# Performance work log

Measured on AMD Instinct MI355X. Metric: run time of the kernel, lower is better.

## Reference

```python
import jax, jax.numpy as jnp
import numpy as np

BN_EPS = 1e-5


def setup_inputs() -> dict:
    key = jax.random.key(0)
    k0, k1, kw, kb, kg, kbe = jax.random.split(key, 6)
    N, L0, L1, D, H = 2, 512, 512, 128, 64
    z0 = jax.random.normal(k0, (N, L0, D), dtype=jnp.float32)
    z1 = jax.random.normal(k1, (N, L1, D), dtype=jnp.float32)
    # Conv2d(2D, H, 1) weight (H, 2D, 1, 1) -> stored as (H, 2D); PyTorch kaiming-uniform-ish init
    bound = 1.0 / np.sqrt(2 * D)
    conv_w = jax.random.uniform(kw, (H, 2 * D), minval=-bound, maxval=bound, dtype=jnp.float32)
    conv_b = jax.random.uniform(kb, (H,), minval=-bound, maxval=bound, dtype=jnp.float32)
    bn_gamma = jnp.ones((H,), dtype=jnp.float32)
    bn_beta = jnp.zeros((H,), dtype=jnp.float32)
    return {"z0": z0, "z1": z1, "conv_w": conv_w, "conv_b": conv_b,
            "bn_gamma": bn_gamma, "bn_beta": bn_beta}


def reference(z0, z1, conv_w, conv_b, bn_gamma, bn_beta):
    # z0: (N, L0, D), z1: (N, L1, D)
    z0t = jnp.transpose(z0, (0, 2, 1))  # (N, D, L0)
    z1t = jnp.transpose(z1, (0, 2, 1))  # (N, D, L1)
    a = z0t[:, :, :, None]              # (N, D, L0, 1)
    b = z1t[:, :, None, :]              # (N, D, 1, L1)
    z_dif = jnp.abs(a - b)              # (N, D, L0, L1)
    z_mul = a * b                       # (N, D, L0, L1)
    z_cat = jnp.concatenate([z_dif, z_mul], axis=1)  # (N, 2D, L0, L1)
    # 1x1 conv == channel contraction
    y = jnp.einsum('ncxy,hc->nhxy', z_cat, conv_w) + conv_b[None, :, None, None]
    y = jax.nn.elu(y)
    # BatchNorm2d, training mode (batch statistics over N, L0, L1 per channel)
    mean = jnp.mean(y, axis=(0, 2, 3), keepdims=True)
    var = jnp.var(y, axis=(0, 2, 3), keepdims=True)
    y = (y - mean) * jax.lax.rsqrt(var + BN_EPS)
    y = y * bn_gamma[None, :, None, None] + bn_beta[None, :, None, None]
    return y
```

## Files before the change

kernel.cpp:

```cpp
#include <hip/hip_runtime.h>

#define NBATCH 2
#define LL 512
#define DDIM 128
#define HCH 64
#define NBLOCKS 1024

typedef float f32x4 __attribute__((ext_vector_type(4)));
typedef __bf16 bf16x8 __attribute__((ext_vector_type(8)));

__device__ __forceinline__ float elu_f(float v) {
  return v > 0.0f ? v : (__expf(v) - 1.0f);
}

__global__ void wprep_kernel(const float* __restrict__ w, bf16x8* __restrict__ wf) {
  int s = blockIdx.x * 256 + threadIdx.x;
  int ck = s >> 8;
  int rem = s & 255;
  int ht = rem >> 6;
  int l = rem & 63;
  int h = ht * 16 + (l & 15);
  int c = ck * 32 + ((l >> 4) << 3);
  const float* src = w + h * 256 + c;
  bf16x8 v;
#pragma unroll
  for (int j = 0; j < 8; ++j) v[j] = (__bf16)src[j];
  wf[s] = v;
}

__device__ __forceinline__ int swz(int i) { return i ^ ((i >> 4) & 7); }

template <int PASS>
__global__ __launch_bounds__(256, 2) void fused_kernel(
    const float* __restrict__ z0g, const float* __restrict__ z1g,
    const bf16x8* __restrict__ wf, const float* __restrict__ cb,
    const float* __restrict__ sstab, float* __restrict__ partials,
    float* __restrict__ out) {
  __shared__ float z0_lds[16 * 128];
  __shared__ f32x4 z1f[1024];
  __shared__ float sred[128];
  __shared__ float cb_lds[64];
  __shared__ float sc_lds[128];

  const int t = threadIdx.x;
  const int lane = t & 63;
  const int wv = t >> 6;
  const int bid = blockIdx.x;
  const int by = bid & 15, bx = (bid >> 4) & 31, n = bid >> 9;
  const int x0 = bx * 16, y0 = by * 32;

  {
    int r = t >> 4, cs = t & 15;
    const f32x4* g0 = (const f32x4*)(z0g + (size_t)(n * LL + x0 + r) * DDIM + cs * 8);
    f32x4 a0 = g0[0], a1 = g0[1];
    ((f32x4*)z0_lds)[r * 32 + cs * 2 + 0] = a0;
    ((f32x4*)z0_lds)[r * 32 + cs * 2 + 1] = a1;
#pragma unroll
    for (int s = t; s < 512; s += 256) {
      int rr = s >> 4, cs1 = s & 15;
      const f32x4* g1 = (const f32x4*)(z1g + (size_t)(n * LL + y0 + rr) * DDIM + cs1 * 8);
      f32x4 b0 = g1[0], b1 = g1[1];
      int yt = rr >> 4, rl = rr & 15, ck = cs1 >> 2, gg = cs1 & 3, fl = gg * 16 + rl;
      int i0 = ((0 * 2 + yt) * 4 + ck) * 64 + fl;
      int i1 = ((1 * 2 + yt) * 4 + ck) * 64 + fl;
      z1f[swz(i0)] = b0;
      z1f[swz(i1)] = b1;
    }
    if (t < 128) sred[t] = 0.0f;
    if (t < 64) cb_lds[t] = cb[t];
    if (PASS == 1 && t < 128) sc_lds[t] = sstab[t];
  }
  __syncthreads();

  f32x4 acc[4][4][2];
  const f32x4 zero4 = {0.f, 0.f, 0.f, 0.f};
#pragma unroll
  for (int xi = 0; xi < 4; ++xi)
#pragma unroll
    for (int ht = 0; ht < 4; ++ht)
#pragma unroll
      for (int yt = 0; yt < 2; ++yt) acc[xi][ht][yt] = zero4;

#pragma unroll
  for (int ckz = 0; ckz < 4; ++ckz) {
    bf16x8 afd[4], afm[4];
#pragma unroll
    for (int ht = 0; ht < 4; ++ht) {
      afd[ht] = wf[(ckz * 4 + ht) * 64 + lane];
      afm[ht] = wf[((ckz + 4) * 4 + ht) * 64 + lane];
    }
    f32x4 b0[2], b1[2];
#pragma unroll
    for (int yt = 0; yt < 2; ++yt) {
      b0[yt] = z1f[swz(((0 * 2 + yt) * 4 + ckz) * 64 + lane)];
      b1[yt] = z1f[swz(((1 * 2 + yt) * 4 + ckz) * 64 + lane)];
    }
#pragma unroll
    for (int xi = 0; xi < 4; ++xi) {
      const int xl = wv * 4 + xi;
      const f32x4* z0p = (const f32x4*)&z0_lds[xl * 128 + ckz * 32 + ((lane >> 4) << 3)];
      f32x4 a0 = z0p[0], a1 = z0p[1];
#pragma unroll
      for (int yt = 0; yt < 2; ++yt) {
        bf16x8 bd, bm;
#pragma unroll
        for (int j = 0; j < 4; ++j) {
          bd[j] = (__bf16)fabsf(a0[j] - b0[yt][j]);
          bd[4 + j] = (__bf16)fabsf(a1[j] - b1[yt][j]);
          bm[j] = (__bf16)(a0[j] * b0[yt][j]);
          bm[4 + j] = (__bf16)(a1[j] * b1[yt][j]);
        }
#pragma unroll
        for (int ht = 0; ht < 4; ++ht) {
          acc[xi][ht][yt] =
              __builtin_amdgcn_mfma_f32_16x16x32_bf16(afd[ht], bd, acc[xi][ht][yt], 0, 0, 0);
          acc[xi][ht][yt] =
              __builtin_amdgcn_mfma_f32_16x16x32_bf16(afm[ht], bm, acc[xi][ht][yt], 0, 0, 0);
        }
      }
    }
  }

  if (PASS == 0) {
    float s1[4][4], s2[4][4];
#pragma unroll
    for (int ht = 0; ht < 4; ++ht)
#pragma unroll
      for (int i = 0; i < 4; ++i) { s1[ht][i] = 0.f; s2[ht][i] = 0.f; }
#pragma unroll
    for (int xi = 0; xi < 4; ++xi)
#pragma unroll
      for (int ht = 0; ht < 4; ++ht)
#pragma unroll
        for (int yt = 0; yt < 2; ++yt)
#pragma unroll
          for (int i = 0; i < 4; ++i) {
            int h = ht * 16 + ((lane >> 4) << 2) + i;
            float v = elu_f(acc[xi][ht][yt][i] + cb_lds[h]);
            s1[ht][i] += v;
            s2[ht][i] += v * v;
          }
#pragma unroll
    for (int ht = 0; ht < 4; ++ht)
#pragma unroll
      for (int i = 0; i < 4; ++i) {
#pragma unroll
        for (int m = 1; m <= 8; m <<= 1) {
          s1[ht][i] += __shfl_xor(s1[ht][i], m, 64);
          s2[ht][i] += __shfl_xor(s2[ht][i], m, 64);
        }
        if ((lane & 15) == 0) {
          int h = ht * 16 + ((lane >> 4) << 2) + i;
          atomicAdd(&sred[h], s1[ht][i]);
          atomicAdd(&sred[64 + h], s2[ht][i]);
        }
      }
    __syncthreads();
    if (t < 128) partials[(size_t)bid * 128 + t] = sred[t];
  } else {
#pragma unroll
    for (int xi = 0; xi < 4; ++xi) {
      const int x = x0 + wv * 4 + xi;
#pragma unroll
      for (int ht = 0; ht < 4; ++ht)
#pragma unroll
        for (int i = 0; i < 4; ++i) {
          int h = ht * 16 + ((lane >> 4) << 2) + i;
          float sc = sc_lds[h], sh = sc_lds[64 + h];
          float* p = out + ((size_t)(n * HCH + h) * LL + x) * LL + y0 + (lane & 15);
          float v0 = elu_f(acc[xi][ht][0][i] + cb_lds[h]);
          float v1 = elu_f(acc[xi][ht][1][i] + cb_lds[h]);
          p[0] = v0 * sc + sh;
          p[16] = v1 * sc + sh;
        }
    }
  }
}

__global__ void bn_finalize_kernel(const float* __restrict__ partials,
                                   const float* __restrict__ gamma,
                                   const float* __restrict__ beta,
                                   float* __restrict__ sstab) {
  const int h = blockIdx.x, t = threadIdx.x;
  const int lane = t & 63, wv = t >> 6;
  float s1 = 0.f, s2 = 0.f;
  for (int b = t; b < NBLOCKS; b += 256) {
    s1 += partials[(size_t)b * 128 + h];
    s2 += partials[(size_t)b * 128 + 64 + h];
  }
#pragma unroll
  for (int m = 1; m <= 32; m <<= 1) {
    s1 += __shfl_xor(s1, m, 64);
    s2 += __shfl_xor(s2, m, 64);
  }
  __shared__ float r1[4], r2[4];
  if (lane == 0) { r1[wv] = s1; r2[wv] = s2; }
  __syncthreads();
  if (t == 0) {
    float S1 = r1[0] + r1[1] + r1[2] + r1[3];
    float S2 = r2[0] + r2[1] + r2[2] + r2[3];
    const float M = 524288.0f;
    float mean = S1 / M;
    float var = S2 / M - mean * mean;
    var = var < 0.f ? 0.f : var;
    float sc = gamma[h] * rsqrtf(var + 1e-5f);
    sstab[h] = sc;
    sstab[64 + h] = beta[h] - mean * sc;
  }
}

extern "C" void kernel_launch(void* const* d_in, const int* in_sizes, int n_in,
                              void* d_out, int out_size, void* d_ws, size_t ws_size,
                              hipStream_t stream) {
  (void)in_sizes; (void)n_in; (void)out_size; (void)ws_size;
  const float* z0 = (const float*)d_in[0];
  const float* z1 = (const float*)d_in[1];
  const float* w = (const float*)d_in[2];
  const float* cb = (const float*)d_in[3];
  const float* gamma = (const float*)d_in[4];
  const float* beta = (const float*)d_in[5];
  float* out = (float*)d_out;

  char* ws = (char*)d_ws;
  bf16x8* wf = (bf16x8*)ws;
  float* partials = (float*)(ws + 32768);
  float* sstab = (float*)(ws + 32768 + NBLOCKS * 128 * 4);

  wprep_kernel<<<8, 256, 0, stream>>>(w, wf);
  fused_kernel<0><<<NBLOCKS, 256, 0, stream>>>(z0, z1, wf, cb, nullptr, partials, nullptr);
  bn_finalize_kernel<<<64, 256, 0, stream>>>(partials, gamma, beta, sstab);
  fused_kernel<1><<<NBLOCKS, 256, 0, stream>>>(z0, z1, wf, cb, sstab, partials, out);
}
```

Measured before the change: 204.1 us.

## Cache ELU activations as bf16 instead of recomputing the conv in a second pass

The second fused conv pass is replaced by a bf16 intermediate buffer written during the stats pass, followed by a simple elementwise BN-apply kernel that reads it back. The stats kernel also halves its x-tile so the grid doubles to 2048 blocks. This removes the duplicated MFMA work but adds a 64 MB bf16 write and read through memory. Output precision drops slightly because the activations are rounded to bf16 before normalization.

```diff
diff --git a/kernel.cpp b/kernel.cpp
--- a/kernel.cpp
+++ b/kernel.cpp
@@ -1,10 +1,9 @@
 #include <hip/hip_runtime.h>
 
-#define NBATCH 2
 #define LL 512
 #define DDIM 128
 #define HCH 64
-#define NBLOCKS 1024
+#define NBLK0 2048
 
 typedef float f32x4 __attribute__((ext_vector_type(4)));
 typedef __bf16 bf16x8 __attribute__((ext_vector_type(8)));
@@ -30,52 +29,45 @@
 
 __device__ __forceinline__ int swz(int i) { return i ^ ((i >> 4) & 7); }
 
-template <int PASS>
-__global__ __launch_bounds__(256, 2) void fused_kernel(
+__global__ __launch_bounds__(256, 2) void conv_stats_kernel(
     const float* __restrict__ z0g, const float* __restrict__ z1g,
     const bf16x8* __restrict__ wf, const float* __restrict__ cb,
-    const float* __restrict__ sstab, float* __restrict__ partials,
-    float* __restrict__ out) {
-  __shared__ float z0_lds[16 * 128];
+    float* __restrict__ partials, __bf16* __restrict__ yb) {
+  __shared__ float z0_lds[8 * 128];
   __shared__ f32x4 z1f[1024];
   __shared__ float sred[128];
   __shared__ float cb_lds[64];
-  __shared__ float sc_lds[128];
 
   const int t = threadIdx.x;
   const int lane = t & 63;
   const int wv = t >> 6;
   const int bid = blockIdx.x;
-  const int by = bid & 15, bx = (bid >> 4) & 31, n = bid >> 9;
-  const int x0 = bx * 16, y0 = by * 32;
-
-  {
+  const int by = bid & 15, bx = (bid >> 4) & 63, n = bid >> 10;
+  const int x0 = bx * 8, y0 = by * 32;
+
+  if (t < 128) {
     int r = t >> 4, cs = t & 15;
     const f32x4* g0 = (const f32x4*)(z0g + (size_t)(n * LL + x0 + r) * DDIM + cs * 8);
-    f32x4 a0 = g0[0], a1 = g0[1];
-    ((f32x4*)z0_lds)[r * 32 + cs * 2 + 0] = a0;
-    ((f32x4*)z0_lds)[r * 32 + cs * 2 + 1] = a1;
-#pragma unroll
-    for (int s = t; s < 512; s += 256) {
-      int rr = s >> 4, cs1 = s & 15;
-      const f32x4* g1 = (const f32x4*)(z1g + (size_t)(n * LL + y0 + rr) * DDIM + cs1 * 8);
-      f32x4 b0 = g1[0], b1 = g1[1];
-      int yt = rr >> 4, rl = rr & 15, ck = cs1 >> 2, gg = cs1 & 3, fl = gg * 16 + rl;
-      int i0 = ((0 * 2 + yt) * 4 + ck) * 64 + fl;
-      int i1 = ((1 * 2 + yt) * 4 + ck) * 64 + fl;
-      z1f[swz(i0)] = b0;
-      z1f[swz(i1)] = b1;
-    }
-    if (t < 128) sred[t] = 0.0f;
-    if (t < 64) cb_lds[t] = cb[t];
-    if (PASS == 1 && t < 128) sc_lds[t] = sstab[t];
-  }
+    ((f32x4*)z0_lds)[r * 32 + cs * 2 + 0] = g0[0];
+    ((f32x4*)z0_lds)[r * 32 + cs * 2 + 1] = g0[1];
+  }
+#pragma unroll
+  for (int s = t; s < 512; s += 256) {
+    int rr = s >> 4, cs1 = s & 15;
+    const f32x4* g1 = (const f32x4*)(z1g + (size_t)(n * LL + y0 + rr) * DDIM + cs1 * 8);
+    f32x4 b0 = g1[0], b1 = g1[1];
+    int yt = rr >> 4, rl = rr & 15, ck = cs1 >> 2, gg = cs1 & 3, fl = gg * 16 + rl;
+    z1f[swz(((0 * 2 + yt) * 4 + ck) * 64 + fl)] = b0;
+    z1f[swz(((1 * 2 + yt) * 4 + ck) * 64 + fl)] = b1;
+  }
+  if (t < 128) sred[t] = 0.0f;
+  if (t < 64) cb_lds[t] = cb[t];
   __syncthreads();
 
-  f32x4 acc[4][4][2];
+  f32x4 acc[2][4][2];
   const f32x4 zero4 = {0.f, 0.f, 0.f, 0.f};
 #pragma unroll
-  for (int xi = 0; xi < 4; ++xi)
+  for (int xi = 0; xi < 2; ++xi)
 #pragma unroll
     for (int ht = 0; ht < 4; ++ht)
 #pragma unroll
@@ -96,8 +88,8 @@
       b1[yt] = z1f[swz(((1 * 2 + yt) * 4 + ckz) * 64 + lane)];
     }
 #pragma unroll
-    for (int xi = 0; xi < 4; ++xi) {
-      const int xl = wv * 4 + xi;
+    for (int xi = 0; xi < 2; ++xi) {
+      const int xl = wv * 2 + xi;
       const f32x4* z0p = (const f32x4*)&z0_lds[xl * 128 + ckz * 32 + ((lane >> 4) << 3)];
       f32x4 a0 = z0p[0], a1 = z0p[1];
 #pragma unroll
@@ -121,60 +113,45 @@
     }
   }
 
-  if (PASS == 0) {
-    float s1[4][4], s2[4][4];
+  float s1[4][4], s2[4][4];
+#pragma unroll
+  for (int ht = 0; ht < 4; ++ht)
+#pragma unroll
+    for (int i = 0; i < 4; ++i) { s1[ht][i] = 0.f; s2[ht][i] = 0.f; }
+#pragma unroll
+  for (int xi = 0; xi < 2; ++xi) {
+    const int x = x0 + wv * 2 + xi;
 #pragma unroll
     for (int ht = 0; ht < 4; ++ht)
 #pragma unroll
-      for (int i = 0; i < 4; ++i) { s1[ht][i] = 0.f; s2[ht][i] = 0.f; }
-#pragma unroll
-    for (int xi = 0; xi < 4; ++xi)
-#pragma unroll
-      for (int ht = 0; ht < 4; ++ht)
-#pragma unroll
-        for (int yt = 0; yt < 2; ++yt)
-#pragma unroll
-          for (int i = 0; i < 4; ++i) {
-            int h = ht * 16 + ((lane >> 4) << 2) + i;
-            float v = elu_f(acc[xi][ht][yt][i] + cb_lds[h]);
-            s1[ht][i] += v;
-            s2[ht][i] += v * v;
-          }
-#pragma unroll
-    for (int ht = 0; ht < 4; ++ht)
-#pragma unroll
       for (int i = 0; i < 4; ++i) {
-#pragma unroll
-        for (int m = 1; m <= 8; m <<= 1) {
-          s1[ht][i] += __shfl_xor(s1[ht][i], m, 64);
-          s2[ht][i] += __shfl_xor(s2[ht][i], m, 64);
-        }
-        if ((lane & 15) == 0) {
-          int h = ht * 16 + ((lane >> 4) << 2) + i;
-          atomicAdd(&sred[h], s1[ht][i]);
-          atomicAdd(&sred[64 + h], s2[ht][i]);
-        }
-      }
-    __syncthreads();
-    if (t < 128) partials[(size_t)bid * 128 + t] = sred[t];
-  } else {
-#pragma unroll
-    for (int xi = 0; xi < 4; ++xi) {
-      const int x = x0 + wv * 4 + xi;
-#pragma unroll
-      for (int ht = 0; ht < 4; ++ht)
-#pragma unroll
-        for (int i = 0; i < 4; ++i) {
-          int h = ht * 16 + ((lane >> 4) << 2) + i;
-          float sc = sc_lds[h], sh = sc_lds[64 + h];
-          float* p = out + ((size_t)(n * HCH + h) * LL + x) * LL + y0 + (lane & 15);
-          float v0 = elu_f(acc[xi][ht][0][i] + cb_lds[h]);
-          float v1 = elu_f(acc[xi][ht][1][i] + cb_lds[h]);
-          p[0] = v0 * sc + sh;
-          p[16] = v1 * sc + sh;
-        }
-    }
-  }
+        int h = ht * 16 + ((lane >> 4) << 2) + i;
+        float v0 = elu_f(acc[xi][ht][0][i] + cb_lds[h]);
+        float v1 = elu_f(acc[xi][ht][1][i] + cb_lds[h]);
+        s1[ht][i] += v0 + v1;
+        s2[ht][i] += v0 * v0 + v1 * v1;
+        __bf16* p = yb + ((size_t)(n * HCH + h) * LL + x) * LL + y0 + (lane & 15);
+        p[0] = (__bf16)v0;
+        p[16] = (__bf16)v1;
+      }
+  }
+#pragma unroll
+  for (int ht = 0; ht < 4; ++ht)
+#pragma unroll
+    for (int i = 0; i < 4; ++i) {
+#pragma unroll
+      for (int m = 1; m <= 8; m <<= 1) {
+        s1[ht][i] += __shfl_xor(s1[ht][i], m, 64);
+        s2[ht][i] += __shfl_xor(s2[ht][i], m, 64);
+      }
+      if ((lane & 15) == 0) {
+        int h = ht * 16 + ((lane >> 4) << 2) + i;
+        atomicAdd(&sred[h], s1[ht][i]);
+        atomicAdd(&sred[64 + h], s2[ht][i]);
+      }
+    }
+  __syncthreads();
+  if (t < 128) partials[(size_t)bid * 128 + t] = sred[t];
 }
 
 __global__ void bn_finalize_kernel(const float* __restrict__ partials,
@@ -184,7 +161,7 @@
   const int h = blockIdx.x, t = threadIdx.x;
   const int lane = t & 63, wv = t >> 6;
   float s1 = 0.f, s2 = 0.f;
-  for (int b = t; b < NBLOCKS; b += 256) {
+  for (int b = t; b < NBLK0; b += 256) {
     s1 += partials[(size_t)b * 128 + h];
     s2 += partials[(size_t)b * 128 + 64 + h];
   }
@@ -209,6 +186,27 @@
   }
 }
 
+__global__ __launch_bounds__(256) void bn_apply_kernel(const __bf16* __restrict__ yb,
+                                                       const float* __restrict__ sstab,
+                                                       float* __restrict__ out) {
+  const int tid = blockIdx.x * 256 + threadIdx.x;
+#pragma unroll
+  for (int g = 0; g < 8; ++g) {
+    int ch = tid + (g << 19);
+    int h = (ch >> 15) & 63;
+    float sc = sstab[h], sh = sstab[64 + h];
+    bf16x8 v = ((const bf16x8*)yb)[ch];
+    f32x4 o0, o1;
+#pragma unroll
+    for (int j = 0; j < 4; ++j) {
+      o0[j] = (float)v[j] * sc + sh;
+      o1[j] = (float)v[4 + j] * sc + sh;
+    }
+    ((f32x4*)out)[ch * 2 + 0] = o0;
+    ((f32x4*)out)[ch * 2 + 1] = o1;
+  }
+}
+
 extern "C" void kernel_launch(void* const* d_in, const int* in_sizes, int n_in,
                               void* d_out, int out_size, void* d_ws, size_t ws_size,
                               hipStream_t stream) {
@@ -223,11 +221,12 @@
 
   char* ws = (char*)d_ws;
   bf16x8* wf = (bf16x8*)ws;
-  float* partials = (float*)(ws + 32768);
-  float* sstab = (float*)(ws + 32768 + NBLOCKS * 128 * 4);
+  float* partials = (float*)(ws + (32 << 10));
+  float* sstab = (float*)(ws + (32 << 10) + (1 << 20));
+  __bf16* yb = (__bf16*)(ws + (32 << 10) + (1 << 20) + (4 << 10));
 
   wprep_kernel<<<8, 256, 0, stream>>>(w, wf);
-  fused_kernel<0><<<NBLOCKS, 256, 0, stream>>>(z0, z1, wf, cb, nullptr, partials, nullptr);
+  conv_stats_kernel<<<NBLK0, 256, 0, stream>>>(z0, z1, wf, cb, partials, yb);
   bn_finalize_kernel<<<64, 256, 0, stream>>>(partials, gamma, beta, sstab);
-  fused_kernel<1><<<NBLOCKS, 256, 0, stream>>>(z0, z1, wf, cb, sstab, partials, out);
-}
+  bn_apply_kernel<<<2048, 256, 0, stream>>>(yb, sstab, out);
+}
```

New measurement: 214.5 us. 1.05x slower.

## Shrink per-block x tile to 4 rows and quadruple grid for occupancy

Applied to the files above, without the earlier changes.

Each wave now handles one x row instead of four, so per-thread accumulators drop from 32 to 8 vectors and launch bounds request 4 blocks per SM. The grid grows from 1024 to 4096 blocks to cover the same output, with partials buffer enlarged accordingly. This aims to increase occupancy and parallelism, but the z1 tile and weight fragments are now reloaded per 4 x rows instead of 16, reducing reuse and increasing staging traffic and BN partial reduction work.

```diff
diff --git a/kernel.cpp b/kernel.cpp
--- a/kernel.cpp
+++ b/kernel.cpp
@@ -1,10 +1,9 @@
 #include <hip/hip_runtime.h>
 
-#define NBATCH 2
 #define LL 512
 #define DDIM 128
 #define HCH 64
-#define NBLOCKS 1024
+#define NBLK 4096
 
 typedef float f32x4 __attribute__((ext_vector_type(4)));
 typedef __bf16 bf16x8 __attribute__((ext_vector_type(8)));
@@ -31,12 +30,12 @@
 __device__ __forceinline__ int swz(int i) { return i ^ ((i >> 4) & 7); }
 
 template <int PASS>
-__global__ __launch_bounds__(256, 2) void fused_kernel(
+__global__ __launch_bounds__(256, 4) void fused_kernel(
     const float* __restrict__ z0g, const float* __restrict__ z1g,
     const bf16x8* __restrict__ wf, const float* __restrict__ cb,
     const float* __restrict__ sstab, float* __restrict__ partials,
     float* __restrict__ out) {
-  __shared__ float z0_lds[16 * 128];
+  __shared__ float z0_lds[4 * 128];
   __shared__ f32x4 z1f[1024];
   __shared__ float sred[128];
   __shared__ float cb_lds[64];
@@ -46,40 +45,36 @@
   const int lane = t & 63;
   const int wv = t >> 6;
   const int bid = blockIdx.x;
-  const int by = bid & 15, bx = (bid >> 4) & 31, n = bid >> 9;
-  const int x0 = bx * 16, y0 = by * 32;
-
-  {
-    int r = t >> 4, cs = t & 15;
-    const f32x4* g0 = (const f32x4*)(z0g + (size_t)(n * LL + x0 + r) * DDIM + cs * 8);
-    f32x4 a0 = g0[0], a1 = g0[1];
-    ((f32x4*)z0_lds)[r * 32 + cs * 2 + 0] = a0;
-    ((f32x4*)z0_lds)[r * 32 + cs * 2 + 1] = a1;
-#pragma unroll
-    for (int s = t; s < 512; s += 256) {
-      int rr = s >> 4, cs1 = s & 15;
-      const f32x4* g1 = (const f32x4*)(z1g + (size_t)(n * LL + y0 + rr) * DDIM + cs1 * 8);
-      f32x4 b0 = g1[0], b1 = g1[1];
-      int yt = rr >> 4, rl = rr & 15, ck = cs1 >> 2, gg = cs1 & 3, fl = gg * 16 + rl;
-      int i0 = ((0 * 2 + yt) * 4 + ck) * 64 + fl;
-      int i1 = ((1 * 2 + yt) * 4 + ck) * 64 + fl;
-      z1f[swz(i0)] = b0;
-      z1f[swz(i1)] = b1;
-    }
-    if (t < 128) sred[t] = 0.0f;
-    if (t < 64) cb_lds[t] = cb[t];
-    if (PASS == 1 && t < 128) sc_lds[t] = sstab[t];
-  }
+  const int by = bid & 15, bx = (bid >> 4) & 127, n = bid >> 11;
+  const int x0 = bx * 4, y0 = by * 32;
+
+  if (t < 128) {
+    int r = t >> 5, cs = t & 31;
+    const f32x4* g0 = (const f32x4*)(z0g + (size_t)(n * LL + x0 + r) * DDIM + cs * 4);
+    ((f32x4*)z0_lds)[r * 32 + cs] = g0[0];
+  }
+#pragma unroll
+  for (int s = t; s < 512; s += 256) {
+    int rr = s >> 4, cs1 = s & 15;
+    const f32x4* g1 = (const f32x4*)(z1g + (size_t)(n * LL + y0 + rr) * DDIM + cs1 * 8);
+    f32x4 b0 = g1[0], b1 = g1[1];
+    int yt = rr >> 4, rl = rr & 15, ck = cs1 >> 2, gg = cs1 & 3, fl = gg * 16 + rl;
+    z1f[swz(((0 * 2 + yt) * 4 + ck) * 64 + fl)] = b0;
+    z1f[swz(((1 * 2 + yt) * 4 + ck) * 64 + fl)] = b1;
+  }
+  if (t < 128) sred[t] = 0.0f;
+  if (t < 64) cb_lds[t] = cb[t];
+  if (PASS == 1 && t < 128) sc_lds[t] = sstab[t];
   __syncthreads();
 
-  f32x4 acc[4][4][2];
+  f32x4 acc[4][2];
   const f32x4 zero4 = {0.f, 0.f, 0.f, 0.f};
 #pragma unroll
-  for (int xi = 0; xi < 4; ++xi)
-#pragma unroll
-    for (int ht = 0; ht < 4; ++ht)
-#pragma unroll
-      for (int yt = 0; yt < 2; ++yt) acc[xi][ht][yt] = zero4;
+  for (int ht = 0; ht < 4; ++ht)
+#pragma unroll
+    for (int yt = 0; yt < 2; ++yt) acc[ht][yt] = zero4;
+
+  const int xl = wv;
 
 #pragma unroll
   for (int ckz = 0; ckz < 4; ++ckz) {
@@ -95,28 +90,24 @@
       b0[yt] = z1f[swz(((0 * 2 + yt) * 4 + ckz) * 64 + lane)];
       b1[yt] = z1f[swz(((1 * 2 + yt) * 4 + ckz) * 64 + lane)];
     }
-#pragma unroll
-    for (int xi = 0; xi < 4; ++xi) {
-      const int xl = wv * 4 + xi;
-      const f32x4* z0p = (const f32x4*)&z0_lds[xl * 128 + ckz * 32 + ((lane >> 4) << 3)];
-      f32x4 a0 = z0p[0], a1 = z0p[1];
-#pragma unroll
-      for (int yt = 0; yt < 2; ++yt) {
-        bf16x8 bd, bm;
-#pragma unroll
-        for (int j = 0; j < 4; ++j) {
-          bd[j] = (__bf16)fabsf(a0[j] - b0[yt][j]);
-          bd[4 + j] = (__bf16)fabsf(a1[j] - b1[yt][j]);
-          bm[j] = (__bf16)(a0[j] * b0[yt][j]);
-          bm[4 + j] = (__bf16)(a1[j] * b1[yt][j]);
-        }
-#pragma unroll
-        for (int ht = 0; ht < 4; ++ht) {
-          acc[xi][ht][yt] =
-              __builtin_amdgcn_mfma_f32_16x16x32_bf16(afd[ht], bd, acc[xi][ht][yt], 0, 0, 0);
-          acc[xi][ht][yt] =
-              __builtin_amdgcn_mfma_f32_16x16x32_bf16(afm[ht], bm, acc[xi][ht][yt], 0, 0, 0);
-        }
+    const f32x4* z0p = (const f32x4*)&z0_lds[xl * 128 + ckz * 32 + ((lane >> 4) << 3)];
+    f32x4 a0 = z0p[0], a1 = z0p[1];
+#pragma unroll
+    for (int yt = 0; yt < 2; ++yt) {
+      bf16x8 bd, bm;
+#pragma unroll
+      for (int j = 0; j < 4; ++j) {
+        bd[j] = (__bf16)fabsf(a0[j] - b0[yt][j]);
+        bd[4 + j] = (__bf16)fabsf(a1[j] - b1[yt][j]);
+        bm[j] = (__bf16)(a0[j] * b0[yt][j]);
+        bm[4 + j] = (__bf16)(a1[j] * b1[yt][j]);
+      }
+#pragma unroll
+      for (int ht = 0; ht < 4; ++ht) {
+        acc[ht][yt] =
+            __builtin_amdgcn_mfma_f32_16x16x32_bf16(afd[ht], bd, acc[ht][yt], 0, 0, 0);
+        acc[ht][yt] =
+            __builtin_amdgcn_mfma_f32_16x16x32_bf16(afm[ht], bm, acc[ht][yt], 0, 0, 0);
       }
     }
   }
@@ -126,20 +117,13 @@
 #pragma unroll
     for (int ht = 0; ht < 4; ++ht)
 #pragma unroll
-      for (int i = 0; i < 4; ++i) { s1[ht][i] = 0.f; s2[ht][i] = 0.f; }
-#pragma unroll
-    for (int xi = 0; xi < 4; ++xi)
-#pragma unroll
-      for (int ht = 0; ht < 4; ++ht)
-#pragma unroll
-        for (int yt = 0; yt < 2; ++yt)
-#pragma unroll
-          for (int i = 0; i < 4; ++i) {
-            int h = ht * 16 + ((lane >> 4) << 2) + i;
-            float v = elu_f(acc[xi][ht][yt][i] + cb_lds[h]);
-            s1[ht][i] += v;
-            s2[ht][i] += v * v;
-          }
+      for (int i = 0; i < 4; ++i) {
+        int h = ht * 16 + ((lane >> 4) << 2) + i;
+        float v0 = elu_f(acc[ht][0][i] + cb_lds[h]);
+        float v1 = elu_f(acc[ht][1][i] + cb_lds[h]);
+        s1[ht][i] = v0 + v1;
+        s2[ht][i] = v0 * v0 + v1 * v1;
+      }
 #pragma unroll
     for (int ht = 0; ht < 4; ++ht)
 #pragma unroll
@@ -158,22 +142,19 @@
     __syncthreads();
     if (t < 128) partials[(size_t)bid * 128 + t] = sred[t];
   } else {
-#pragma unroll
-    for (int xi = 0; xi < 4; ++xi) {
-      const int x = x0 + wv * 4 + xi;
-#pragma unroll
-      for (int ht = 0; ht < 4; ++ht)
-#pragma unroll
-        for (int i = 0; i < 4; ++i) {
-          int h = ht * 16 + ((lane >> 4) << 2) + i;
-          float sc = sc_lds[h], sh = sc_lds[64 + h];
-          float* p = out + ((size_t)(n * HCH + h) * LL + x) * LL + y0 + (lane & 15);
-          float v0 = elu_f(acc[xi][ht][0][i] + cb_lds[h]);
-          float v1 = elu_f(acc[xi][ht][1][i] + cb_lds[h]);
-          p[0] = v0 * sc + sh;
-          p[16] = v1 * sc + sh;
-        }
-    }
+    const int x = x0 + wv;
+#pragma unroll
+    for (int ht = 0; ht < 4; ++ht)
+#pragma unroll
+      for (int i = 0; i < 4; ++i) {
+        int h = ht * 16 + ((lane >> 4) << 2) + i;
+        float sc = sc_lds[h], sh = sc_lds[64 + h];
+        float* p = out + ((size_t)(n * HCH + h) * LL + x) * LL + y0 + (lane & 15);
+        float v0 = elu_f(acc[ht][0][i] + cb_lds[h]);
+        float v1 = elu_f(acc[ht][1][i] + cb_lds[h]);
+        p[0] = v0 * sc + sh;
+        p[16] = v1 * sc + sh;
+      }
   }
 }
 
@@ -184,7 +165,7 @@
   const int h = blockIdx.x, t = threadIdx.x;
   const int lane = t & 63, wv = t >> 6;
   float s1 = 0.f, s2 = 0.f;
-  for (int b = t; b < NBLOCKS; b += 256) {
+  for (int b = t; b < NBLK; b += 256) {
     s1 += partials[(size_t)b * 128 + h];
     s2 += partials[(size_t)b * 128 + 64 + h];
   }
@@ -223,11 +204,11 @@
 
   char* ws = (char*)d_ws;
   bf16x8* wf = (bf16x8*)ws;
-  float* partials = (float*)(ws + 32768);
-  float* sstab = (float*)(ws + 32768 + NBLOCKS * 128 * 4);
+  float* partials = (float*)(ws + (64 << 10));
+  float* sstab = (float*)(ws + (64 << 10) + (2 << 20));
 
   wprep_kernel<<<8, 256, 0, stream>>>(w, wf);
-  fused_kernel<0><<<NBLOCKS, 256, 0, stream>>>(z0, z1, wf, cb, nullptr, partials, nullptr);
+  fused_kernel<0><<<NBLK, 256, 0, stream>>>(z0, z1, wf, cb, nullptr, partials, nullptr);
   bn_finalize_kernel<<<64, 256, 0, stream>>>(partials, gamma, beta, sstab);
-  fused_kernel<1><<<NBLOCKS, 256, 0, stream>>>(z0, z1, wf, cb, sstab, partials, out);
-}
+  fused_kernel<1><<<NBLK, 256, 0, stream>>>(z0, z1, wf, cb, sstab, partials, out);
+}
```

New measurement: 212.7 us. +4.3%, slower.
